# Kernel tuning notes

Measured on AMD Instinct MI355X. Metric: run time of the kernel, lower is better.

Reference implementation:

```python
import jax, jax.numpy as jnp
import numpy as np

BATCH = 4096
DIM = 512
TEMP = 0.1

def setup_inputs() -> dict:
    key = jax.random.key(0)
    k1, k2 = jax.random.split(key)
    emb_i = jax.random.normal(k1, (BATCH, DIM), dtype=jnp.float32)
    emb_j = jax.random.normal(k2, (BATCH, DIM), dtype=jnp.float32)
    return {"emb_i": emb_i, "emb_j": emb_j}

def _l2_normalize(x, eps=1e-12):
    # matches torch F.normalize(dim=1): x / max(||x||, eps)
    norm = jnp.sqrt(jnp.sum(x * x, axis=1, keepdims=True))
    return x / jnp.maximum(norm, eps)

def reference(emb_i, emb_j):
    n = emb_i.shape[0]
    z_i = _l2_normalize(emb_i)
    z_j = _l2_normalize(emb_j)
    reps = jnp.concatenate([z_i, z_j], axis=0)  # [2N, D], rows unit-norm
    # cosine similarity of unit vectors == dot product -> GEMM instead of O(N^2 D) broadcast
    sim = reps @ reps.T  # [2N, 2N]
    # positives: diag offsets +N and -N
    pos_ij = jnp.sum(z_i * z_j, axis=1)  # diag(sim, +N)
    pos_ji = pos_ij                      # diag(sim, -N) is identical by symmetry
    positives = jnp.concatenate([pos_ij, pos_ji], axis=0)  # [2N]
    nominator = jnp.exp(positives / TEMP)
    neg_mask = 1.0 - jnp.eye(2 * n, dtype=sim.dtype)
    denominator = jnp.sum(neg_mask * jnp.exp(sim / TEMP), axis=1)  # [2N]
    loss_partial = -jnp.log(nominator / denominator)
    return jnp.sum(loss_partial) / (2 * n)
```

## Files before the change

### kernel.cpp

```cpp
#include <hip/hip_runtime.h>
#include <hip/hip_bf16.h>
#include <math.h>

#define N_ROWS 4096
#define DIM    512
#define M_ROWS 8192
#define BK     32
#define NTILES 64
#define NBLOCKS 2080
#define EXP_SCALE 14.4269504088896340736f

typedef unsigned short ushort_t;
typedef __attribute__((ext_vector_type(8))) short short8;
typedef __attribute__((ext_vector_type(4))) float f32x4;

__device__ __forceinline__ ushort_t f2bf(float x) {
  unsigned int bits = __float_as_uint(x);
  unsigned int lsb = (bits >> 16) & 1u;
  bits += 0x7fffu + lsb;
  return (ushort_t)(bits >> 16);
}

__device__ __forceinline__ void store4bf(ushort_t* p, float4 v, float s) {
  union { ushort_t u[4]; uint2 d; } pk;
  pk.u[0] = f2bf(v.x * s);
  pk.u[1] = f2bf(v.y * s);
  pk.u[2] = f2bf(v.z * s);
  pk.u[3] = f2bf(v.w * s);
  *(uint2*)p = pk.d;
}

__device__ __forceinline__ void async16(const ushort_t* g, ushort_t* l) {
  __builtin_amdgcn_global_load_lds(
      (const __attribute__((address_space(1))) void*)g,
      (__attribute__((address_space(3))) void*)l,
      16, 0, 0);
}

__global__ __launch_bounds__(64) void norm_kernel(
    const float* __restrict__ ei, const float* __restrict__ ej,
    ushort_t* __restrict__ reps, float* __restrict__ pos,
    float* __restrict__ denom) {
  int b = blockIdx.x;
  int lane = threadIdx.x;
  if (lane == 0) {
    denom[b] = 0.0f;
    denom[b + N_ROWS] = 0.0f;
  }
  const float4* pi = (const float4*)(ei + (size_t)b * DIM);
  const float4* pj = (const float4*)(ej + (size_t)b * DIM);
  float4 a0 = pi[lane];
  float4 a1 = pi[lane + 64];
  float4 b0 = pj[lane];
  float4 b1 = pj[lane + 64];

  float si = a0.x*a0.x + a0.y*a0.y + a0.z*a0.z + a0.w*a0.w
           + a1.x*a1.x + a1.y*a1.y + a1.z*a1.z + a1.w*a1.w;
  float sj = b0.x*b0.x + b0.y*b0.y + b0.z*b0.z + b0.w*b0.w
           + b1.x*b1.x + b1.y*b1.y + b1.z*b1.z + b1.w*b1.w;
  float dp = a0.x*b0.x + a0.y*b0.y + a0.z*b0.z + a0.w*b0.w
           + a1.x*b1.x + a1.y*b1.y + a1.z*b1.z + a1.w*b1.w;

#pragma unroll
  for (int m = 32; m >= 1; m >>= 1) {
    si += __shfl_xor(si, m, 64);
    sj += __shfl_xor(sj, m, 64);
    dp += __shfl_xor(dp, m, 64);
  }
  float ii = 1.0f / fmaxf(sqrtf(si), 1e-12f);
  float ij = 1.0f / fmaxf(sqrtf(sj), 1e-12f);
  if (lane == 0) pos[b] = dp * ii * ij;

  ushort_t* ri = reps + (size_t)b * DIM;
  ushort_t* rj = reps + (size_t)(b + N_ROWS) * DIM;
  store4bf(ri + lane * 4,       a0, ii);
  store4bf(ri + 256 + lane * 4, a1, ii);
  store4bf(rj + lane * 4,       b0, ij);
  store4bf(rj + 256 + lane * 4, b1, ij);
}

__global__ __launch_bounds__(256) void sim_kernel(
    const ushort_t* __restrict__ reps, float* __restrict__ denom) {
  int id = blockIdx.x;
  id = (id & 7) * (NBLOCKS / 8) + (id >> 3);
  int bj = (int)((sqrtf(8.0f * (float)id + 1.0f) - 1.0f) * 0.5f);
  while ((bj + 1) * (bj + 2) / 2 <= id) ++bj;
  while (bj * (bj + 1) / 2 > id) --bj;
  int bi = id - bj * (bj + 1) / 2;

  __shared__ ushort_t As[2][128 * BK];
  __shared__ ushort_t Bs[2][128 * BK];

  int tid  = threadIdx.x;
  int wave = tid >> 6, lane = tid & 63;
  int wr = wave >> 1, wc = wave & 1;
  int quad = lane >> 4, l15 = lane & 15;

  int c0 = wave * 2, c1 = c0 + 1;
  int srow  = lane >> 2;
  int selem = ((lane & 3) ^ ((srow >> 1) & 3)) * 8;
  const ushort_t* gA0 = reps + (size_t)(bi * 128 + c0 * 16 + srow) * DIM + selem;
  const ushort_t* gA1 = reps + (size_t)(bi * 128 + c1 * 16 + srow) * DIM + selem;
  const ushort_t* gB0 = reps + (size_t)(bj * 128 + c0 * 16 + srow) * DIM + selem;
  const ushort_t* gB1 = reps + (size_t)(bj * 128 + c1 * 16 + srow) * DIM + selem;

  f32x4 zero4 = {0.0f, 0.0f, 0.0f, 0.0f};
  f32x4 acc[4][4];
#pragma unroll
  for (int tr = 0; tr < 4; ++tr)
#pragma unroll
    for (int tc = 0; tc < 4; ++tc) acc[tr][tc] = zero4;

  int sqr = (quad ^ ((l15 >> 1) & 3)) * 8;

  async16(gA0, &As[0][c0 * 512]);
  async16(gA1, &As[0][c1 * 512]);
  async16(gB0, &Bs[0][c0 * 512]);
  async16(gB1, &Bs[0][c1 * 512]);
  __syncthreads();

  int cur = 0;
  for (int kk = 0; kk < DIM; kk += BK) {
    int nxt = cur ^ 1;
    if (kk + BK < DIM) {
      async16(gA0 + kk + BK, &As[nxt][c0 * 512]);
      async16(gA1 + kk + BK, &As[nxt][c1 * 512]);
      async16(gB0 + kk + BK, &Bs[nxt][c0 * 512]);
      async16(gB1 + kk + BK, &Bs[nxt][c1 * 512]);
    }

    short8 aF[4], bF[4];
#pragma unroll
    for (int t = 0; t < 4; ++t) {
      aF[t] = *(const short8*)(&As[cur][(wr * 64 + t * 16 + l15) * BK + sqr]);
      bF[t] = *(const short8*)(&Bs[cur][(wc * 64 + t * 16 + l15) * BK + sqr]);
    }
#pragma unroll
    for (int tr = 0; tr < 4; ++tr)
#pragma unroll
      for (int tc = 0; tc < 4; ++tc)
        acc[tr][tc] = __builtin_amdgcn_mfma_f32_16x16x32_bf16(
            aF[tr], bF[tc], acc[tr][tc], 0, 0, 0);

    __syncthreads();
    cur = nxt;
  }

  int rowg_base = bi * 128 + wr * 64;
  int colg_base = bj * 128 + wc * 64;

  f32x4 rsum[4];
  float csum[4] = {0.0f, 0.0f, 0.0f, 0.0f};
#pragma unroll
  for (int tr = 0; tr < 4; ++tr) rsum[tr] = zero4;

#pragma unroll
  for (int tr = 0; tr < 4; ++tr) {
    int rowg0 = rowg_base + tr * 16 + quad * 4;
#pragma unroll
    for (int tc = 0; tc < 4; ++tc) {
      int colg = colg_base + tc * 16 + l15;
      f32x4 a = acc[tr][tc];
      f32x4 e;
#pragma unroll
      for (int r = 0; r < 4; ++r) {
        float v = exp2f(a[r] * EXP_SCALE);
        e[r] = ((rowg0 + r) == colg) ? 0.0f : v;
      }
      rsum[tr] += e;
      csum[tc] += e[0] + e[1] + e[2] + e[3];
    }
  }

#pragma unroll
  for (int m = 1; m <= 8; m <<= 1)
#pragma unroll
    for (int tr = 0; tr < 4; ++tr)
#pragma unroll
      for (int r = 0; r < 4; ++r)
        rsum[tr][r] += __shfl_xor(rsum[tr][r], m, 64);

  if (l15 == 0) {
#pragma unroll
    for (int tr = 0; tr < 4; ++tr)
#pragma unroll
      for (int r = 0; r < 4; ++r)
        atomicAdd(&denom[rowg_base + tr * 16 + quad * 4 + r], rsum[tr][r]);
  }

  if (bi != bj) {
#pragma unroll
    for (int m = 16; m <= 32; m <<= 1)
#pragma unroll
      for (int tc = 0; tc < 4; ++tc)
        csum[tc] += __shfl_xor(csum[tc], m, 64);
    if (quad == 0) {
#pragma unroll
      for (int tc = 0; tc < 4; ++tc)
        atomicAdd(&denom[colg_base + tc * 16 + l15], csum[tc]);
    }
  }
}

__global__ __launch_bounds__(256) void loss_kernel(
    const float* __restrict__ denom, const float* __restrict__ pos,
    float* __restrict__ out) {
  __shared__ float red[4];
  int tid = threadIdx.x;
  float p = 0.0f;
  for (int r = tid; r < M_ROWS; r += 256)
    p += logf(denom[r]) - pos[r & (N_ROWS - 1)] * 10.0f;
#pragma unroll
  for (int m = 32; m >= 1; m >>= 1) p += __shfl_xor(p, m, 64);
  if ((tid & 63) == 0) red[tid >> 6] = p;
  __syncthreads();
  if (tid == 0)
    out[0] = (red[0] + red[1] + red[2] + red[3]) * (1.0f / M_ROWS);
}

extern "C" void kernel_launch(void* const* d_in, const int* in_sizes, int n_in,
                              void* d_out, int out_size, void* d_ws, size_t ws_size,
                              hipStream_t stream) {
  const float* ei = (const float*)d_in[0];
  const float* ej = (const float*)d_in[1];
  float* out = (float*)d_out;

  char* ws = (char*)d_ws;
  ushort_t* reps = (ushort_t*)ws;
  float* denom = (float*)(ws + (size_t)M_ROWS * DIM * 2);
  float* pos = (float*)(ws + (size_t)M_ROWS * DIM * 2 + M_ROWS * 4);

  norm_kernel<<<N_ROWS, 64, 0, stream>>>(ei, ej, reps, pos, denom);
  sim_kernel<<<NBLOCKS, 256, 0, stream>>>(reps, denom);
  loss_kernel<<<1, 256, 0, stream>>>(denom, pos, out);
}
```

Baseline: 146.2 us.

## Supertile tile ordering, single-barrier pipelined K loop, wider norm and loss blocks

```diff
diff --git a/kernel.cpp b/kernel.cpp
--- a/kernel.cpp
+++ b/kernel.cpp
@@ -6,8 +6,9 @@
 #define DIM    512
 #define M_ROWS 8192
 #define BK     32
-#define NTILES 64
-#define NBLOCKS 2080
+#define NTILE  64
+#define NB     2080
+#define NSTEP  16
 #define EXP_SCALE 14.4269504088896340736f
 
 typedef unsigned short ushort_t;
@@ -37,12 +38,13 @@
       16, 0, 0);
 }
 
-__global__ __launch_bounds__(64) void norm_kernel(
+__global__ __launch_bounds__(256) void norm_kernel(
     const float* __restrict__ ei, const float* __restrict__ ej,
     ushort_t* __restrict__ reps, float* __restrict__ pos,
     float* __restrict__ denom) {
-  int b = blockIdx.x;
-  int lane = threadIdx.x;
+  int wave = threadIdx.x >> 6;
+  int lane = threadIdx.x & 63;
+  int b = blockIdx.x * 4 + wave;
   if (lane == 0) {
     denom[b] = 0.0f;
     denom[b + N_ROWS] = 0.0f;
@@ -82,11 +84,28 @@
 __global__ __launch_bounds__(256) void sim_kernel(
     const ushort_t* __restrict__ reps, float* __restrict__ denom) {
   int id = blockIdx.x;
-  id = (id & 7) * (NBLOCKS / 8) + (id >> 3);
-  int bj = (int)((sqrtf(8.0f * (float)id + 1.0f) - 1.0f) * 0.5f);
-  while ((bj + 1) * (bj + 2) / 2 <= id) ++bj;
-  while (bj * (bj + 1) / 2 > id) --bj;
-  int bi = id - bj * (bj + 1) / 2;
+  id = (id & 7) * (NB / 8) + (id >> 3);
+
+  int bi, bj;
+  {
+    int rem = id, Si = 0, Sj = 0, fnd = 0;
+    for (int s_j = 0; s_j < 4 && !fnd; ++s_j)
+      for (int s_i = 0; s_i <= s_j && !fnd; ++s_i) {
+        int sz = (s_i == s_j) ? 136 : 256;
+        if (rem < sz) { Si = s_i; Sj = s_j; fnd = 1; }
+        else rem -= sz;
+      }
+    if (Si == Sj) {
+      int tj = 0;
+      while ((tj + 1) * (tj + 2) / 2 <= rem) ++tj;
+      int ti = rem - tj * (tj + 1) / 2;
+      bi = Si * 16 + ti;
+      bj = Sj * 16 + tj;
+    } else {
+      bi = Si * 16 + (rem & 15);
+      bj = Sj * 16 + (rem >> 4);
+    }
+  }
 
   __shared__ ushort_t As[2][128 * BK];
   __shared__ ushort_t Bs[2][128 * BK];
@@ -104,6 +123,15 @@
   const ushort_t* gB0 = reps + (size_t)(bj * 128 + c0 * 16 + srow) * DIM + selem;
   const ushort_t* gB1 = reps + (size_t)(bj * 128 + c1 * 16 + srow) * DIM + selem;
 
+#define STAGE(D, KOFF) do {                         \
+    async16(gA0 + (KOFF), &As[D][c0 * 512]);        \
+    async16(gA1 + (KOFF), &As[D][c1 * 512]);        \
+    async16(gB0 + (KOFF), &Bs[D][c0 * 512]);        \
+    async16(gB1 + (KOFF), &Bs[D][c1 * 512]);        \
+  } while (0)
+
+  int sqr = (quad ^ ((l15 >> 1) & 3)) * 8;
+
   f32x4 zero4 = {0.0f, 0.0f, 0.0f, 0.0f};
   f32x4 acc[4][4];
 #pragma unroll
@@ -111,23 +139,15 @@
 #pragma unroll
     for (int tc = 0; tc < 4; ++tc) acc[tr][tc] = zero4;
 
-  int sqr = (quad ^ ((l15 >> 1) & 3)) * 8;
-
-  async16(gA0, &As[0][c0 * 512]);
-  async16(gA1, &As[0][c1 * 512]);
-  async16(gB0, &Bs[0][c0 * 512]);
-  async16(gB1, &Bs[0][c1 * 512]);
-  __syncthreads();
-
-  int cur = 0;
-  for (int kk = 0; kk < DIM; kk += BK) {
-    int nxt = cur ^ 1;
-    if (kk + BK < DIM) {
-      async16(gA0 + kk + BK, &As[nxt][c0 * 512]);
-      async16(gA1 + kk + BK, &As[nxt][c1 * 512]);
-      async16(gB0 + kk + BK, &Bs[nxt][c0 * 512]);
-      async16(gB1 + kk + BK, &Bs[nxt][c1 * 512]);
-    }
+  STAGE(0, 0);
+
+  for (int kk = 0; kk < NSTEP; ++kk) {
+    int cur = kk & 1;
+    int nk = ((kk + 1) & 15) * BK;
+
+    STAGE(cur ^ 1, nk);
+    asm volatile("s_waitcnt vmcnt(4)" ::: "memory");
+    __builtin_amdgcn_s_barrier();
 
     short8 aF[4], bF[4];
 #pragma unroll
@@ -135,16 +155,17 @@
       aF[t] = *(const short8*)(&As[cur][(wr * 64 + t * 16 + l15) * BK + sqr]);
       bF[t] = *(const short8*)(&Bs[cur][(wc * 64 + t * 16 + l15) * BK + sqr]);
     }
+    __builtin_amdgcn_s_setprio(1);
 #pragma unroll
     for (int tr = 0; tr < 4; ++tr)
 #pragma unroll
       for (int tc = 0; tc < 4; ++tc)
         acc[tr][tc] = __builtin_amdgcn_mfma_f32_16x16x32_bf16(
             aF[tr], bF[tc], acc[tr][tc], 0, 0, 0);
-
-    __syncthreads();
-    cur = nxt;
-  }
+    __builtin_amdgcn_s_setprio(0);
+    __builtin_amdgcn_s_barrier();
+  }
+  asm volatile("s_waitcnt vmcnt(0)" ::: "memory");
 
   int rowg_base = bi * 128 + wr * 64;
   int colg_base = bj * 128 + wc * 64;
@@ -202,20 +223,24 @@
   }
 }
 
-__global__ __launch_bounds__(256) void loss_kernel(
+__global__ __launch_bounds__(1024) void loss_kernel(
     const float* __restrict__ denom, const float* __restrict__ pos,
     float* __restrict__ out) {
-  __shared__ float red[4];
+  __shared__ float red[16];
   int tid = threadIdx.x;
   float p = 0.0f;
-  for (int r = tid; r < M_ROWS; r += 256)
+  for (int r = tid; r < M_ROWS; r += 1024)
     p += logf(denom[r]) - pos[r & (N_ROWS - 1)] * 10.0f;
 #pragma unroll
   for (int m = 32; m >= 1; m >>= 1) p += __shfl_xor(p, m, 64);
   if ((tid & 63) == 0) red[tid >> 6] = p;
   __syncthreads();
-  if (tid == 0)
-    out[0] = (red[0] + red[1] + red[2] + red[3]) * (1.0f / M_ROWS);
+  if (tid == 0) {
+    float s = 0.0f;
+#pragma unroll
+    for (int i = 0; i < 16; ++i) s += red[i];
+    out[0] = s * (1.0f / M_ROWS);
+  }
 }
 
 extern "C" void kernel_launch(void* const* d_in, const int* in_sizes, int n_in,
@@ -230,7 +255,7 @@
   float* denom = (float*)(ws + (size_t)M_ROWS * DIM * 2);
   float* pos = (float*)(ws + (size_t)M_ROWS * DIM * 2 + M_ROWS * 4);
 
-  norm_kernel<<<N_ROWS, 64, 0, stream>>>(ei, ej, reps, pos, denom);
-  sim_kernel<<<NBLOCKS, 256, 0, stream>>>(reps, denom);
-  loss_kernel<<<1, 256, 0, stream>>>(denom, pos, out);
-}
+  norm_kernel<<<N_ROWS / 4, 256, 0, stream>>>(ei, ej, reps, pos, denom);
+  sim_kernel<<<NB, 256, 0, stream>>>(reps, denom);
+  loss_kernel<<<1, 1024, 0, stream>>>(denom, pos, out);
+}
```

After: 136.2 us. 1.07x faster.
